# Kernel optimization log

Hardware: AMD Instinct MI355X
Metric: run time of the kernel (lower is better)

## Reference

```python
import jax, jax.numpy as jnp
import numpy as np

C = 256
C8 = C // 8

def setup_inputs() -> dict:
    key = jax.random.key(0)
    ks = jax.random.split(key, 8)
    B, H, W = 4, 64, 64
    x = jax.random.normal(ks[0], (B, C, H, W), dtype=jnp.float32)
    wq = jax.random.normal(ks[1], (C8, C), dtype=jnp.float32) * (1.0 / np.sqrt(C))
    bq = jnp.zeros((C8,), dtype=jnp.float32)
    wk = jax.random.normal(ks[2], (C8, C), dtype=jnp.float32) * (1.0 / np.sqrt(C))
    bk = jnp.zeros((C8,), dtype=jnp.float32)
    wv = jax.random.normal(ks[3], (C, C), dtype=jnp.float32) * (1.0 / np.sqrt(C))
    bv = jnp.zeros((C,), dtype=jnp.float32)
    gamma = jnp.ones((1,), dtype=jnp.float32) * 0.5  # nonzero so attention path contributes
    return {"x": x, "wq": wq, "bq": bq, "wk": wk, "bk": bk, "wv": wv, "bv": bv, "gamma": gamma}

def reference(x, wq, bq, wk, bk, wv, bv, gamma):
    B, Cc, Hh, Ww = x.shape
    N = Hh * Ww
    xf = x.reshape(B, Cc, N)  # [B,C,N]
    # 1x1 convs == per-pixel linear maps
    q = jnp.einsum('oc,bcn->bon', wq, xf) + bq[None, :, None]  # [B,C8,N]
    k = jnp.einsum('oc,bcn->bon', wk, xf) + bk[None, :, None]  # [B,C8,N]
    v = jnp.einsum('oc,bcn->bon', wv, xf) + bv[None, :, None]  # [B,C,N]
    # energy[b,n,m] = sum_c q[b,c,n] * k[b,c,m]  (unscaled)
    energy = jnp.einsum('bcn,bcm->bnm', q, k)
    attn = jax.nn.softmax(energy, axis=-1)
    # out[b,c,n] = sum_m v[b,c,m] * attn[b,n,m]
    out = jnp.einsum('bcm,bnm->bcn', v, attn).reshape(B, Cc, Hh, Ww)
    return gamma * out + x
```

## Files before the change

### kernel.cpp

```cpp
#include <hip/hip_runtime.h>
#include <hip/hip_fp16.h>

#define CC   256
#define QKC  32
#define NPIX 4096
#define NB   4
#define XSTR 264
#define VSTR 72
#define LOG2E 1.44269504088896340736f
#define TAU  8.0f

typedef __attribute__((ext_vector_type(8))) _Float16 f16x8;
typedef __attribute__((ext_vector_type(4))) float     f32x4;

static __device__ __forceinline__ unsigned h2bits(__half2 h) {
    union { __half2 h; unsigned u; } cv; cv.h = h; return cv.u;
}
#define E2(x) __builtin_amdgcn_exp2f(x)

__global__ __launch_bounds__(256) void wh_prep(
    const float* __restrict__ wq, const float* __restrict__ wk,
    const float* __restrict__ wv, __half* __restrict__ Wh)
{
    const int idx4 = blockIdx.x * 256 + threadIdx.x;
    const int o  = idx4 >> 6;
    const int cw = (idx4 & 63) << 2;
    const float* src;
    float scale = 1.0f;
    if (o < 256)      src = wv + (size_t)o * 256 + cw;
    else if (o < 288) { src = wq + (size_t)(o - 256) * 256 + cw; scale = LOG2E; }
    else              src = wk + (size_t)(o - 288) * 256 + cw;
    const float4 v = *reinterpret_cast<const float4*>(src);
    __half h[4] = {__float2half(v.x * scale), __float2half(v.y * scale),
                   __float2half(v.z * scale), __float2half(v.w * scale)};
    *reinterpret_cast<uint2*>(Wh + (size_t)o * 256 + cw) =
        *reinterpret_cast<const uint2*>(h);
}

__global__ __launch_bounds__(512) void qkv_mfma(
    const float* __restrict__ x, const __half* __restrict__ Wh,
    const float* __restrict__ bq, const float* __restrict__ bk,
    const float* __restrict__ bv,
    __half* __restrict__ Qh, __half* __restrict__ Kh, __half* __restrict__ VTh)
{
    __shared__ __align__(16) __half sm[CC * VSTR];
    __half* xT   = sm;
    __half* vres = sm;

    const int t  = threadIdx.x;
    const int b  = blockIdx.x >> 6;
    const int n0 = (blockIdx.x & 63) << 6;

    {
        const int nl4 = t & 15;
        const int c0  = t >> 4;
        const float* xp = x + ((size_t)b * CC) * NPIX + n0 + nl4 * 4;
        #pragma unroll
        for (int i = 0; i < 8; ++i) {
            const int c = c0 + 32 * i;
            const float4 v = *reinterpret_cast<const float4*>(xp + (size_t)c * NPIX);
            xT[(nl4 * 4 + 0) * XSTR + c] = __float2half(v.x);
            xT[(nl4 * 4 + 1) * XSTR + c] = __float2half(v.y);
            xT[(nl4 * 4 + 2) * XSTR + c] = __float2half(v.z);
            xT[(nl4 * 4 + 3) * XSTR + c] = __float2half(v.w);
        }
    }
    __syncthreads();

    const int w = t >> 6, l = t & 63, lr = l & 15, s = l >> 4;
    const int nto = (w < 4) ? 3 : 2;
    const int ob0 = 32 * w, ob1 = 32 * w + 16, ob2 = 256 + 16 * w;

    f16x8 wf[3][8];
    #pragma unroll
    for (int kk = 0; kk < 8; ++kk) {
        wf[0][kk] = *reinterpret_cast<const f16x8*>(
            Wh + (size_t)(ob0 + lr) * 256 + kk * 32 + s * 8);
        wf[1][kk] = *reinterpret_cast<const f16x8*>(
            Wh + (size_t)(ob1 + lr) * 256 + kk * 32 + s * 8);
    }
    if (w < 4)
        #pragma unroll
        for (int kk = 0; kk < 8; ++kk)
            wf[2][kk] = *reinterpret_cast<const f16x8*>(
                Wh + (size_t)(ob2 + lr) * 256 + kk * 32 + s * 8);

    f32x4 acc[3][4];
    #pragma unroll
    for (int j = 0; j < 3; ++j)
        #pragma unroll
        for (int nt = 0; nt < 4; ++nt) acc[j][nt] = (f32x4){0.f, 0.f, 0.f, 0.f};

    #pragma unroll
    for (int nt = 0; nt < 4; ++nt) {
        f16x8 xf[8];
        #pragma unroll
        for (int kk = 0; kk < 8; ++kk)
            xf[kk] = *reinterpret_cast<const f16x8*>(
                &xT[(nt * 16 + lr) * XSTR + kk * 32 + s * 8]);
        #pragma unroll
        for (int j = 0; j < 3; ++j)
            if (j < nto)
                #pragma unroll
                for (int kk = 0; kk < 8; ++kk)
                    acc[j][nt] = __builtin_amdgcn_mfma_f32_16x16x32_f16(
                        xf[kk], wf[j][kk], acc[j][nt], 0, 0, 0);
    }

    if (w < 4) {
        const bool is_q = (w < 2);
        const int oc = (w & 1) * 16 + lr;
        __half* dst = is_q ? Qh : Kh;
        const float bias = is_q ? bq[oc] * LOG2E : bk[oc];
        #pragma unroll
        for (int nt = 0; nt < 4; ++nt)
            #pragma unroll
            for (int r = 0; r < 4; ++r) {
                const size_t n = (size_t)b * NPIX + n0 + nt * 16 + s * 4 + r;
                dst[n * QKC + oc] = __float2half(acc[2][nt][r] + bias);
            }
    }

    __syncthreads();
    {
        #pragma unroll
        for (int j = 0; j < 2; ++j) {
            const int c = 32 * w + 16 * j + lr;
            const float bias = bv[c];
            #pragma unroll
            for (int nt = 0; nt < 4; ++nt) {
                __half h[4];
                #pragma unroll
                for (int r = 0; r < 4; ++r) h[r] = __float2half(acc[j][nt][r] + bias);
                *reinterpret_cast<uint2*>(&vres[c * VSTR + nt * 16 + s * 4]) =
                    *reinterpret_cast<const uint2*>(h);
            }
        }
    }
    __syncthreads();
    {
        const int c = t >> 1, half = t & 1;
        __half* dst = VTh + ((size_t)(b * CC + c)) * NPIX + n0 + half * 32;
        #pragma unroll
        for (int jj = 0; jj < 4; ++jj)
            *reinterpret_cast<uint4*>(dst + jj * 8) =
                *reinterpret_cast<const uint4*>(&vres[c * VSTR + half * 32 + jj * 8]);
    }
}

__global__ __launch_bounds__(512) void attn_mfma(
    const __half* __restrict__ Qh, const __half* __restrict__ Kh,
    const __half* __restrict__ VTh, const float* __restrict__ x,
    const float* __restrict__ gamma, float* __restrict__ out)
{
    __shared__ unsigned char Praw[2][64 * 128];
    __shared__ float abuf[2][64];
    __shared__ __align__(16) int fbuf[2][4];
    __shared__ float lbuf[64];

    const int t  = threadIdx.x;
    const int w  = t >> 6;
    const int l  = t & 63;
    const int lr = l & 15;
    const int s  = l >> 4;

    const int blk = (blockIdx.x & 7) * 32 + (blockIdx.x >> 3);
    const int b  = blk >> 6;
    const int n0 = (blk & 63) << 6;

    const int qw = w * 16 + lr;
    f16x8 qfrag;
    f16x8 kf[4];
    float m_run = -1e30f, l_run = 0.f;
    const __half* kbase = Kh + ((size_t)b * NPIX + lr) * QKC + s * 8;

    const int cbase = 64 * (w - 4);
    const __half* vbase = VTh + ((size_t)(b * CC + cbase + lr)) * NPIX + s * 8;
    f16x8 vA[4][2], vB[4][2];
    f32x4 O[4][4];
    #pragma unroll
    for (int ct = 0; ct < 4; ++ct)
        #pragma unroll
        for (int qt = 0; qt < 4; ++qt)
            O[ct][qt] = (f32x4){0.f, 0.f, 0.f, 0.f};

    auto do_softmax = [&](int bw) {
        f32x4 sacc[4];
        #pragma unroll
        for (int mt = 0; mt < 4; ++mt)
            sacc[mt] = __builtin_amdgcn_mfma_f32_16x16x32_f16(
                kf[mt], qfrag, (f32x4){0.f, 0.f, 0.f, 0.f}, 0, 0, 0);
        float v[16];
        #pragma unroll
        for (int mt = 0; mt < 4; ++mt)
            #pragma unroll
            for (int r = 0; r < 4; ++r) v[mt * 4 + r] = sacc[mt][r];
        float t8[8], t4[4], t2[2];
        #pragma unroll
        for (int i = 0; i < 8; ++i) t8[i] = fmaxf(v[i], v[i + 8]);
        #pragma unroll
        for (int i = 0; i < 4; ++i) t4[i] = fmaxf(t8[i], t8[i + 4]);
        t2[0] = fmaxf(t4[0], t4[2]); t2[1] = fmaxf(t4[1], t4[3]);
        const float m_l = fmaxf(t2[0], t2[1]);
        float p[16];
        #pragma unroll
        for (int i = 0; i < 16; ++i) p[i] = E2(v[i] - m_l);
        float s8[8], s4[4], s2[2];
        #pragma unroll
        for (int i = 0; i < 8; ++i) s8[i] = p[i] + p[i + 8];
        #pragma unroll
        for (int i = 0; i < 4; ++i) s4[i] = s8[i] + s8[i + 4];
        s2[0] = s4[0] + s4[2]; s2[1] = s4[1] + s4[3];
        const float e_l = s2[0] + s2[1];
        float m_p = __shfl_xor(m_l, 16);
        float e_p = __shfl_xor(e_l, 16);
        const float m1 = fmaxf(m_l, m_p);
        const float e1 = e_l * E2(m_l - m1) + e_p * E2(m_p - m1);
        m_p = __shfl_xor(m1, 32);
        e_p = __shfl_xor(e1, 32);
        const float m_g = fmaxf(m1, m_p);
        const float e_g = e1 * E2(m1 - m_g) + e_p * E2(m_p - m_g);
        const bool need = (m_g - m_run) > TAU;
        float f;
        if (__any(need)) {
            const float mnew = fmaxf(m_run, m_g);
            const float al   = E2(m_run - mnew);
            l_run = al * l_run + e_g * E2(m_g - mnew);
            f = E2(m_l - mnew);
            if (l < 16) abuf[bw][qw] = al;
            if (l == 0) fbuf[bw][w] = 1;
            m_run = mnew;
        } else {
            l_run += e_g * E2(m_g - m_run);
            f = E2(m_l - m_run);
            if (l < 16) abuf[bw][qw] = 1.0f;
            if (l == 0) fbuf[bw][w] = 0;
        }
        unsigned char* pb = &Praw[bw][0];
        #pragma unroll
        for (int mt = 0; mt < 4; ++mt) {
            const int g = ((s >> 1) + 2 * mt) ^ (qw & 7);
            uint2 u;
            u.x = h2bits(__floats2half2_rn(p[mt * 4 + 0] * f, p[mt * 4 + 1] * f));
            u.y = h2bits(__floats2half2_rn(p[mt * 4 + 2] * f, p[mt * 4 + 3] * f));
            *reinterpret_cast<uint2*>(pb + qw * 128 + g * 16 + (s & 1) * 8) = u;
        }
    };

    auto vload = [&](f16x8 (&dst)[4][2], int m0) {
        #pragma unroll
        for (int ct = 0; ct < 4; ++ct)
            #pragma unroll
            for (int ks = 0; ks < 2; ++ks)
                dst[ct][ks] = *reinterpret_cast<const f16x8*>(
                    vbase + (size_t)ct * 16 * NPIX + m0 + ks * 32);
    };

    auto pv_body = [&](int pbuf, f16x8 (&vf)[4][2]) {
        const int4 fl = *reinterpret_cast<const int4*>(&fbuf[pbuf][0]);
        if (fl.x | fl.y | fl.z | fl.w) {
            float av[4];
            #pragma unroll
            for (int qt = 0; qt < 4; ++qt) av[qt] = abuf[pbuf][qt * 16 + lr];
            #pragma unroll
            for (int ct = 0; ct < 4; ++ct)
                #pragma unroll
                for (int qt = 0; qt < 4; ++qt)
                    #pragma unroll
                    for (int r = 0; r < 4; ++r) O[ct][qt][r] *= av[qt];
        }
        const unsigned char* pr = &Praw[pbuf][0];
        __builtin_amdgcn_s_setprio(1);
        #pragma unroll
        for (int qt = 0; qt < 4; ++qt) {
            const int q2 = qt * 16 + lr;
            const int g0 = s ^ (q2 & 7);
            const int g1 = (s + 4) ^ (q2 & 7);
            const f16x8 pf0 = *reinterpret_cast<const f16x8*>(pr + q2 * 128 + g0 * 16);
            const f16x8 pf1 = *reinterpret_cast<const f16x8*>(pr + q2 * 128 + g1 * 16);
            #pragma unroll
            for (int ct = 0; ct < 4; ++ct) {
                O[ct][qt] = __builtin_amdgcn_mfma_f32_16x16x32_f16(
                    vf[ct][0], pf0, O[ct][qt], 0, 0, 0);
                O[ct][qt] = __builtin_amdgcn_mfma_f32_16x16x32_f16(
                    vf[ct][1], pf1, O[ct][qt], 0, 0, 0);
            }
        }
        __builtin_amdgcn_s_setprio(0);
    };

    if (w < 4) {
        qfrag = *reinterpret_cast<const f16x8*>(
            Qh + ((size_t)b * NPIX + n0 + qw) * QKC + s * 8);
        #pragma unroll
        for (int mt = 0; mt < 4; ++mt)
            kf[mt] = *reinterpret_cast<const f16x8*>(kbase + (size_t)(mt * 16) * QKC);
        do_softmax(0);
        #pragma unroll
        for (int mt = 0; mt < 4; ++mt)
            kf[mt] = *reinterpret_cast<const f16x8*>(kbase + (size_t)(64 + mt * 16) * QKC);
    } else {
        vload(vA, 0);
    }
    __syncthreads();

    for (int it = 0; it < 32; ++it) {
        const int se = 2 * it;
        if (w < 4) {
            do_softmax(1);
            if (se < 62) {
                const size_t moff = (size_t)((se + 2) * 64) * QKC;
                #pragma unroll
                for (int mt = 0; mt < 4; ++mt)
                    kf[mt] = *reinterpret_cast<const f16x8*>(
                        kbase + moff + (size_t)(mt * 16) * QKC);
            }
        } else {
            vload(vB, (se + 1) * 64);
            pv_body(0, vA);
        }
        __syncthreads();
        const int so = se + 1;
        if (w < 4) {
            if (so < 63) {
                do_softmax(0);
                if (so < 62) {
                    const size_t moff = (size_t)((so + 2) * 64) * QKC;
                    #pragma unroll
                    for (int mt = 0; mt < 4; ++mt)
                        kf[mt] = *reinterpret_cast<const f16x8*>(
                            kbase + moff + (size_t)(mt * 16) * QKC);
                }
            }
        } else {
            if (so < 63) vload(vA, (so + 1) * 64);
            pv_body(1, vB);
        }
        __syncthreads();
    }

    if (w < 4) { if (l < 16) lbuf[qw] = l_run; }
    __syncthreads();
    if (w >= 4) {
        const float g = gamma[0];
        float linv[4];
        #pragma unroll
        for (int qt = 0; qt < 4; ++qt) linv[qt] = g / lbuf[qt * 16 + lr];
        #pragma unroll
        for (int ct = 0; ct < 4; ++ct)
            #pragma unroll
            for (int qt = 0; qt < 4; ++qt)
                #pragma unroll
                for (int r = 0; r < 4; ++r) {
                    const int c = cbase + ct * 16 + s * 4 + r;
                    const size_t idx = ((size_t)(b * CC + c)) * NPIX + n0 + qt * 16 + lr;
                    out[idx] = O[ct][qt][r] * linv[qt] + x[idx];
                }
    }
}

extern "C" void kernel_launch(void* const* d_in, const int* in_sizes, int n_in,
                              void* d_out, int out_size, void* d_ws, size_t ws_size,
                              hipStream_t stream) {
    const float* x     = (const float*)d_in[0];
    const float* wq    = (const float*)d_in[1];
    const float* bq    = (const float*)d_in[2];
    const float* wk    = (const float*)d_in[3];
    const float* bk    = (const float*)d_in[4];
    const float* wv    = (const float*)d_in[5];
    const float* bv    = (const float*)d_in[6];
    const float* gamma = (const float*)d_in[7];
    float* out = (float*)d_out;

    __half* Wh  = (__half*)d_ws;
    __half* Qh  = Wh + (size_t)320 * 256;
    __half* Kh  = Qh + (size_t)NB * NPIX * QKC;
    __half* VTh = Kh + (size_t)NB * NPIX * QKC;

    hipLaunchKernelGGL(wh_prep, dim3(80), dim3(256), 0, stream, wq, wk, wv, Wh);
    hipLaunchKernelGGL(qkv_mfma, dim3(NB * 64), dim3(512), 0, stream,
                       x, Wh, bq, bk, bv, Qh, Kh, VTh);
    hipLaunchKernelGGL(attn_mfma, dim3(256), dim3(512), 0, stream,
                       Qh, Kh, VTh, x, gamma, out);
}
```

Baseline: 108.2 us.

## Split PV work across eight consumer waves with 128-key softmax intervals

```diff
diff --git a/kernel.cpp b/kernel.cpp
--- a/kernel.cpp
+++ b/kernel.cpp
@@ -7,6 +7,7 @@
 #define NB   4
 #define XSTR 264
 #define VSTR 72
+#define OSTR 68
 #define LOG2E 1.44269504088896340736f
 #define TAU  8.0f
 
@@ -148,15 +149,18 @@
     }
 }
 
-__global__ __launch_bounds__(512) void attn_mfma(
+__global__ __launch_bounds__(768, 3) void attn_mfma(
     const __half* __restrict__ Qh, const __half* __restrict__ Kh,
     const __half* __restrict__ VTh, const float* __restrict__ x,
     const float* __restrict__ gamma, float* __restrict__ out)
 {
-    __shared__ unsigned char Praw[2][64 * 128];
+    __shared__ __align__(16) unsigned char smraw[4 * 64 * OSTR * 4];
     __shared__ float abuf[2][64];
     __shared__ __align__(16) int fbuf[2][4];
     __shared__ float lbuf[64];
+
+    unsigned char* const Praw = smraw;
+    float* const Ocomb = reinterpret_cast<float*>(smraw);
 
     const int t  = threadIdx.x;
     const int w  = t >> 6;
@@ -170,13 +174,14 @@
 
     const int qw = w * 16 + lr;
     f16x8 qfrag;
-    f16x8 kf[4];
+    f16x8 kfA[4], kfB[4];
     float m_run = -1e30f, l_run = 0.f;
     const __half* kbase = Kh + ((size_t)b * NPIX + lr) * QKC + s * 8;
 
-    const int cbase = 64 * (w - 4);
-    const __half* vbase = VTh + ((size_t)(b * CC + cbase + lr)) * NPIX + s * 8;
-    f16x8 vA[4][2], vB[4][2];
+    const int wid = w - 4;
+    const int cg  = wid & 3;
+    const int mh  = wid >> 2;
+    const __half* vbase = VTh + ((size_t)(b * CC + cg * 64 + lr)) * NPIX + s * 8;
     f32x4 O[4][4];
     #pragma unroll
     for (int ct = 0; ct < 4; ++ct)
@@ -184,84 +189,108 @@
         for (int qt = 0; qt < 4; ++qt)
             O[ct][qt] = (f32x4){0.f, 0.f, 0.f, 0.f};
 
-    auto do_softmax = [&](int bw) {
-        f32x4 sacc[4];
+    auto ldk = [&](f16x8 (&dst)[4], int tile) {
+        const size_t off = (size_t)(tile * 64) * QKC;
         #pragma unroll
         for (int mt = 0; mt < 4; ++mt)
-            sacc[mt] = __builtin_amdgcn_mfma_f32_16x16x32_f16(
-                kf[mt], qfrag, (f32x4){0.f, 0.f, 0.f, 0.f}, 0, 0, 0);
-        float v[16];
+            dst[mt] = *reinterpret_cast<const f16x8*>(
+                kbase + off + (size_t)(mt * 16) * QKC);
+    };
+
+    auto do_interval = [&](int i, int bw) {
+        f32x4 sa[4], sb[4];
         #pragma unroll
         for (int mt = 0; mt < 4; ++mt)
-            #pragma unroll
-            for (int r = 0; r < 4; ++r) v[mt * 4 + r] = sacc[mt][r];
-        float t8[8], t4[4], t2[2];
-        #pragma unroll
-        for (int i = 0; i < 8; ++i) t8[i] = fmaxf(v[i], v[i + 8]);
-        #pragma unroll
-        for (int i = 0; i < 4; ++i) t4[i] = fmaxf(t8[i], t8[i + 4]);
-        t2[0] = fmaxf(t4[0], t4[2]); t2[1] = fmaxf(t4[1], t4[3]);
-        const float m_l = fmaxf(t2[0], t2[1]);
-        float p[16];
-        #pragma unroll
-        for (int i = 0; i < 16; ++i) p[i] = E2(v[i] - m_l);
-        float s8[8], s4[4], s2[2];
-        #pragma unroll
-        for (int i = 0; i < 8; ++i) s8[i] = p[i] + p[i + 8];
-        #pragma unroll
-        for (int i = 0; i < 4; ++i) s4[i] = s8[i] + s8[i + 4];
-        s2[0] = s4[0] + s4[2]; s2[1] = s4[1] + s4[3];
-        const float e_l = s2[0] + s2[1];
-        float m_p = __shfl_xor(m_l, 16);
-        float e_p = __shfl_xor(e_l, 16);
-        const float m1 = fmaxf(m_l, m_p);
-        const float e1 = e_l * E2(m_l - m1) + e_p * E2(m_p - m1);
+            sa[mt] = __builtin_amdgcn_mfma_f32_16x16x32_f16(
+                kfA[mt], qfrag, (f32x4){0.f, 0.f, 0.f, 0.f}, 0, 0, 0);
+        #pragma unroll
+        for (int mt = 0; mt < 4; ++mt)
+            sb[mt] = __builtin_amdgcn_mfma_f32_16x16x32_f16(
+                kfB[mt], qfrag, (f32x4){0.f, 0.f, 0.f, 0.f}, 0, 0, 0);
+        if (i < 31) { ldk(kfA, 2 * i + 2); ldk(kfB, 2 * i + 3); }
+
+        float va[16], vb[16];
+        #pragma unroll
+        for (int mt = 0; mt < 4; ++mt)
+            #pragma unroll
+            for (int r = 0; r < 4; ++r) {
+                va[mt * 4 + r] = sa[mt][r];
+                vb[mt * 4 + r] = sb[mt][r];
+            }
+        float ta[8], tb[8];
+        #pragma unroll
+        for (int i2 = 0; i2 < 8; ++i2) { ta[i2] = fmaxf(va[i2], va[i2+8]); tb[i2] = fmaxf(vb[i2], vb[i2+8]); }
+        float ta4[4], tb4[4];
+        #pragma unroll
+        for (int i2 = 0; i2 < 4; ++i2) { ta4[i2] = fmaxf(ta[i2], ta[i2+4]); tb4[i2] = fmaxf(tb[i2], tb[i2+4]); }
+        const float m_lA = fmaxf(fmaxf(ta4[0], ta4[2]), fmaxf(ta4[1], ta4[3]));
+        const float m_lB = fmaxf(fmaxf(tb4[0], tb4[2]), fmaxf(tb4[1], tb4[3]));
+        float pa[16], pb[16];
+        #pragma unroll
+        for (int i2 = 0; i2 < 16; ++i2) { pa[i2] = E2(va[i2] - m_lA); pb[i2] = E2(vb[i2] - m_lB); }
+        float sa8[8], sb8[8];
+        #pragma unroll
+        for (int i2 = 0; i2 < 8; ++i2) { sa8[i2] = pa[i2] + pa[i2+8]; sb8[i2] = pb[i2] + pb[i2+8]; }
+        float sa4[4], sb4[4];
+        #pragma unroll
+        for (int i2 = 0; i2 < 4; ++i2) { sa4[i2] = sa8[i2] + sa8[i2+4]; sb4[i2] = sb8[i2] + sb8[i2+4]; }
+        const float e_lA = (sa4[0] + sa4[2]) + (sa4[1] + sa4[3]);
+        const float e_lB = (sb4[0] + sb4[2]) + (sb4[1] + sb4[3]);
+        const float m_ab = fmaxf(m_lA, m_lB);
+        const float e_ab = e_lA * E2(m_lA - m_ab) + e_lB * E2(m_lB - m_ab);
+        float m_p = __shfl_xor(m_ab, 16);
+        float e_p = __shfl_xor(e_ab, 16);
+        const float m1 = fmaxf(m_ab, m_p);
+        const float e1 = e_ab * E2(m_ab - m1) + e_p * E2(m_p - m1);
         m_p = __shfl_xor(m1, 32);
         e_p = __shfl_xor(e1, 32);
         const float m_g = fmaxf(m1, m_p);
         const float e_g = e1 * E2(m1 - m_g) + e_p * E2(m_p - m_g);
         const bool need = (m_g - m_run) > TAU;
-        float f;
+        float fA, fB;
         if (__any(need)) {
             const float mnew = fmaxf(m_run, m_g);
             const float al   = E2(m_run - mnew);
             l_run = al * l_run + e_g * E2(m_g - mnew);
-            f = E2(m_l - mnew);
+            fA = E2(m_lA - mnew); fB = E2(m_lB - mnew);
             if (l < 16) abuf[bw][qw] = al;
             if (l == 0) fbuf[bw][w] = 1;
             m_run = mnew;
         } else {
             l_run += e_g * E2(m_g - m_run);
-            f = E2(m_l - m_run);
+            fA = E2(m_lA - m_run); fB = E2(m_lB - m_run);
             if (l < 16) abuf[bw][qw] = 1.0f;
             if (l == 0) fbuf[bw][w] = 0;
         }
-        unsigned char* pb = &Praw[bw][0];
+        unsigned char* pbA = Praw + bw * 16384;
+        unsigned char* pbB = pbA + 8192;
         #pragma unroll
         for (int mt = 0; mt < 4; ++mt) {
             const int g = ((s >> 1) + 2 * mt) ^ (qw & 7);
-            uint2 u;
-            u.x = h2bits(__floats2half2_rn(p[mt * 4 + 0] * f, p[mt * 4 + 1] * f));
-            u.y = h2bits(__floats2half2_rn(p[mt * 4 + 2] * f, p[mt * 4 + 3] * f));
-            *reinterpret_cast<uint2*>(pb + qw * 128 + g * 16 + (s & 1) * 8) = u;
+            uint2 ua, ub;
+            ua.x = h2bits(__floats2half2_rn(pa[mt*4+0] * fA, pa[mt*4+1] * fA));
+            ua.y = h2bits(__floats2half2_rn(pa[mt*4+2] * fA, pa[mt*4+3] * fA));
+            ub.x = h2bits(__floats2half2_rn(pb[mt*4+0] * fB, pb[mt*4+1] * fB));
+            ub.y = h2bits(__floats2half2_rn(pb[mt*4+2] * fB, pb[mt*4+3] * fB));
+            *reinterpret_cast<uint2*>(pbA + qw * 128 + g * 16 + (s & 1) * 8) = ua;
+            *reinterpret_cast<uint2*>(pbB + qw * 128 + g * 16 + (s & 1) * 8) = ub;
         }
     };
 
-    auto vload = [&](f16x8 (&dst)[4][2], int m0) {
+    auto pv = [&](int i, int bw) {
+        const int m0 = i * 128 + mh * 64;
+        f16x8 vf[4][2];
         #pragma unroll
         for (int ct = 0; ct < 4; ++ct)
             #pragma unroll
             for (int ks = 0; ks < 2; ++ks)
-                dst[ct][ks] = *reinterpret_cast<const f16x8*>(
+                vf[ct][ks] = *reinterpret_cast<const f16x8*>(
                     vbase + (size_t)ct * 16 * NPIX + m0 + ks * 32);
-    };
-
-    auto pv_body = [&](int pbuf, f16x8 (&vf)[4][2]) {
-        const int4 fl = *reinterpret_cast<const int4*>(&fbuf[pbuf][0]);
+        const int4 fl = *reinterpret_cast<const int4*>(&fbuf[bw][0]);
         if (fl.x | fl.y | fl.z | fl.w) {
             float av[4];
             #pragma unroll
-            for (int qt = 0; qt < 4; ++qt) av[qt] = abuf[pbuf][qt * 16 + lr];
+            for (int qt = 0; qt < 4; ++qt) av[qt] = abuf[bw][qt * 16 + lr];
             #pragma unroll
             for (int ct = 0; ct < 4; ++ct)
                 #pragma unroll
@@ -269,7 +298,7 @@
                     #pragma unroll
                     for (int r = 0; r < 4; ++r) O[ct][qt][r] *= av[qt];
         }
-        const unsigned char* pr = &Praw[pbuf][0];
+        const unsigned char* pr = Praw + bw * 16384 + mh * 8192;
         __builtin_amdgcn_s_setprio(1);
         #pragma unroll
         for (int qt = 0; qt < 4; ++qt) {
@@ -292,69 +321,50 @@
     if (w < 4) {
         qfrag = *reinterpret_cast<const f16x8*>(
             Qh + ((size_t)b * NPIX + n0 + qw) * QKC + s * 8);
-        #pragma unroll
-        for (int mt = 0; mt < 4; ++mt)
-            kf[mt] = *reinterpret_cast<const f16x8*>(kbase + (size_t)(mt * 16) * QKC);
-        do_softmax(0);
-        #pragma unroll
-        for (int mt = 0; mt < 4; ++mt)
-            kf[mt] = *reinterpret_cast<const f16x8*>(kbase + (size_t)(64 + mt * 16) * QKC);
-    } else {
-        vload(vA, 0);
+        ldk(kfA, 0); ldk(kfB, 1);
+        do_interval(0, 0);
     }
     __syncthreads();
 
     for (int it = 0; it < 32; ++it) {
-        const int se = 2 * it;
         if (w < 4) {
-            do_softmax(1);
-            if (se < 62) {
-                const size_t moff = (size_t)((se + 2) * 64) * QKC;
-                #pragma unroll
-                for (int mt = 0; mt < 4; ++mt)
-                    kf[mt] = *reinterpret_cast<const f16x8*>(
-                        kbase + moff + (size_t)(mt * 16) * QKC);
-            }
+            if (it < 31) do_interval(it + 1, (it + 1) & 1);
         } else {
-            vload(vB, (se + 1) * 64);
-            pv_body(0, vA);
+            pv(it, it & 1);
         }
         __syncthreads();
-        const int so = se + 1;
-        if (w < 4) {
-            if (so < 63) {
-                do_softmax(0);
-                if (so < 62) {
-                    const size_t moff = (size_t)((so + 2) * 64) * QKC;
-                    #pragma unroll
-                    for (int mt = 0; mt < 4; ++mt)
-                        kf[mt] = *reinterpret_cast<const f16x8*>(
-                            kbase + moff + (size_t)(mt * 16) * QKC);
-                }
-            }
-        } else {
-            if (so < 63) vload(vA, (so + 1) * 64);
-            pv_body(1, vB);
-        }
-        __syncthreads();
-    }
-
-    if (w < 4) { if (l < 16) lbuf[qw] = l_run; }
-    __syncthreads();
-    if (w >= 4) {
+    }
+
+    if (w < 4) {
+        if (l < 16) lbuf[qw] = l_run;
+    } else if (mh == 1) {
+        float* oc = Ocomb + cg * 64 * OSTR;
+        #pragma unroll
+        for (int ct = 0; ct < 4; ++ct)
+            #pragma unroll
+            for (int qt = 0; qt < 4; ++qt)
+                #pragma unroll
+                for (int r = 0; r < 4; ++r)
+                    oc[(ct * 16 + s * 4 + r) * OSTR + qt * 16 + lr] = O[ct][qt][r];
+    }
+    __syncthreads();
+    if (w >= 4 && mh == 0) {
         const float g = gamma[0];
         float linv[4];
         #pragma unroll
         for (int qt = 0; qt < 4; ++qt) linv[qt] = g / lbuf[qt * 16 + lr];
+        const float* oc = Ocomb + cg * 64 * OSTR;
         #pragma unroll
         for (int ct = 0; ct < 4; ++ct)
             #pragma unroll
             for (int qt = 0; qt < 4; ++qt)
                 #pragma unroll
                 for (int r = 0; r < 4; ++r) {
-                    const int c = cbase + ct * 16 + s * 4 + r;
+                    const int c = cg * 64 + ct * 16 + s * 4 + r;
                     const size_t idx = ((size_t)(b * CC + c)) * NPIX + n0 + qt * 16 + lr;
-                    out[idx] = O[ct][qt][r] * linv[qt] + x[idx];
+                    const float o2 = O[ct][qt][r] +
+                                     oc[(ct * 16 + s * 4 + r) * OSTR + qt * 16 + lr];
+                    out[idx] = o2 * linv[qt] + x[idx];
                 }
     }
 }
@@ -380,6 +390,6 @@
     hipLaunchKernelGGL(wh_prep, dim3(80), dim3(256), 0, stream, wq, wk, wv, Wh);
     hipLaunchKernelGGL(qkv_mfma, dim3(NB * 64), dim3(512), 0, stream,
                        x, Wh, bq, bk, bv, Qh, Kh, VTh);
-    hipLaunchKernelGGL(attn_mfma, dim3(256), dim3(512), 0, stream,
+    hipLaunchKernelGGL(attn_mfma, dim3(256), dim3(768), 0, stream,
                        Qh, Kh, VTh, x, gamma, out);
 }
```

After: 156.1 us. 44.4% more time.

## Split attention over key range into two halves with a combine kernel

Applied to the files above, without the earlier changes.

```diff
diff --git a/kernel.cpp b/kernel.cpp
--- a/kernel.cpp
+++ b/kernel.cpp
@@ -148,10 +148,10 @@
     }
 }
 
-__global__ __launch_bounds__(512) void attn_mfma(
+__global__ __launch_bounds__(512, 4) void attn_partial(
     const __half* __restrict__ Qh, const __half* __restrict__ Kh,
-    const __half* __restrict__ VTh, const float* __restrict__ x,
-    const float* __restrict__ gamma, float* __restrict__ out)
+    const __half* __restrict__ VTh, float2* __restrict__ ML,
+    __half* __restrict__ Oc1, float* __restrict__ out)
 {
     __shared__ unsigned char Praw[2][64 * 128];
     __shared__ float abuf[2][64];
@@ -164,18 +164,19 @@
     const int lr = l & 15;
     const int s  = l >> 4;
 
-    const int blk = (blockIdx.x & 7) * 32 + (blockIdx.x >> 3);
-    const int b  = blk >> 6;
-    const int n0 = (blk & 63) << 6;
+    const int lb = (blockIdx.x & 7) * 64 + (blockIdx.x >> 3);
+    const int h  = lb >> 8;
+    const int b  = (lb >> 6) & 3;
+    const int n0 = (lb & 63) << 6;
 
     const int qw = w * 16 + lr;
     f16x8 qfrag;
     f16x8 kf[4];
     float m_run = -1e30f, l_run = 0.f;
-    const __half* kbase = Kh + ((size_t)b * NPIX + lr) * QKC + s * 8;
+    const __half* kbase = Kh + ((size_t)b * NPIX + h * 2048 + lr) * QKC + s * 8;
 
     const int cbase = 64 * (w - 4);
-    const __half* vbase = VTh + ((size_t)(b * CC + cbase + lr)) * NPIX + s * 8;
+    const __half* vbase = VTh + ((size_t)(b * CC + cbase + lr)) * NPIX + h * 2048 + s * 8;
     f16x8 vA[4][2], vB[4][2];
     f32x4 O[4][4];
     #pragma unroll
@@ -184,6 +185,14 @@
         for (int qt = 0; qt < 4; ++qt)
             O[ct][qt] = (f32x4){0.f, 0.f, 0.f, 0.f};
 
+    auto ldk = [&](int tile) {
+        const size_t off = (size_t)(tile * 64) * QKC;
+        #pragma unroll
+        for (int mt = 0; mt < 4; ++mt)
+            kf[mt] = *reinterpret_cast<const f16x8*>(
+                kbase + off + (size_t)(mt * 16) * QKC);
+    };
+
     auto do_softmax = [&](int bw) {
         f32x4 sacc[4];
         #pragma unroll
@@ -195,23 +204,21 @@
         for (int mt = 0; mt < 4; ++mt)
             #pragma unroll
             for (int r = 0; r < 4; ++r) v[mt * 4 + r] = sacc[mt][r];
-        float t8[8], t4[4], t2[2];
+        float t8[8], t4[4];
         #pragma unroll
         for (int i = 0; i < 8; ++i) t8[i] = fmaxf(v[i], v[i + 8]);
         #pragma unroll
         for (int i = 0; i < 4; ++i) t4[i] = fmaxf(t8[i], t8[i + 4]);
-        t2[0] = fmaxf(t4[0], t4[2]); t2[1] = fmaxf(t4[1], t4[3]);
-        const float m_l = fmaxf(t2[0], t2[1]);
+        const float m_l = fmaxf(fmaxf(t4[0], t4[2]), fmaxf(t4[1], t4[3]));
         float p[16];
         #pragma unroll
         for (int i = 0; i < 16; ++i) p[i] = E2(v[i] - m_l);
-        float s8[8], s4[4], s2[2];
+        float s8[8], s4[4];
         #pragma unroll
         for (int i = 0; i < 8; ++i) s8[i] = p[i] + p[i + 8];
         #pragma unroll
         for (int i = 0; i < 4; ++i) s4[i] = s8[i] + s8[i + 4];
-        s2[0] = s4[0] + s4[2]; s2[1] = s4[1] + s4[3];
-        const float e_l = s2[0] + s2[1];
+        const float e_l = (s4[0] + s4[2]) + (s4[1] + s4[3]);
         float m_p = __shfl_xor(m_l, 16);
         float e_p = __shfl_xor(e_l, 16);
         const float m1 = fmaxf(m_l, m_p);
@@ -289,74 +296,126 @@
         __builtin_amdgcn_s_setprio(0);
     };
 
+    #define STEP_BARRIER(IS_S)                                    \
+        { if (IS_S) asm volatile("s_waitcnt lgkmcnt(0)" ::: "memory"); \
+          __builtin_amdgcn_sched_barrier(0);                      \
+          __builtin_amdgcn_s_barrier();                           \
+          __builtin_amdgcn_sched_barrier(0); }
+
     if (w < 4) {
         qfrag = *reinterpret_cast<const f16x8*>(
             Qh + ((size_t)b * NPIX + n0 + qw) * QKC + s * 8);
-        #pragma unroll
-        for (int mt = 0; mt < 4; ++mt)
-            kf[mt] = *reinterpret_cast<const f16x8*>(kbase + (size_t)(mt * 16) * QKC);
+        ldk(0);
         do_softmax(0);
-        #pragma unroll
-        for (int mt = 0; mt < 4; ++mt)
-            kf[mt] = *reinterpret_cast<const f16x8*>(kbase + (size_t)(64 + mt * 16) * QKC);
+        ldk(1);
+        STEP_BARRIER(true)
     } else {
         vload(vA, 0);
-    }
-    __syncthreads();
-
-    for (int it = 0; it < 32; ++it) {
+        STEP_BARRIER(false)
+    }
+
+    for (int it = 0; it < 16; ++it) {
         const int se = 2 * it;
         if (w < 4) {
             do_softmax(1);
-            if (se < 62) {
-                const size_t moff = (size_t)((se + 2) * 64) * QKC;
-                #pragma unroll
-                for (int mt = 0; mt < 4; ++mt)
-                    kf[mt] = *reinterpret_cast<const f16x8*>(
-                        kbase + moff + (size_t)(mt * 16) * QKC);
-            }
+            if (se < 30) ldk(se + 2);
+            STEP_BARRIER(true)
         } else {
             vload(vB, (se + 1) * 64);
             pv_body(0, vA);
-        }
-        __syncthreads();
+            STEP_BARRIER(false)
+        }
         const int so = se + 1;
         if (w < 4) {
-            if (so < 63) {
+            if (so < 31) {
                 do_softmax(0);
-                if (so < 62) {
-                    const size_t moff = (size_t)((so + 2) * 64) * QKC;
-                    #pragma unroll
-                    for (int mt = 0; mt < 4; ++mt)
-                        kf[mt] = *reinterpret_cast<const f16x8*>(
-                            kbase + moff + (size_t)(mt * 16) * QKC);
-                }
+                if (so < 30) ldk(so + 2);
             }
+            STEP_BARRIER(true)
         } else {
-            if (so < 63) vload(vA, (so + 1) * 64);
+            if (so < 31) vload(vA, (so + 1) * 64);
             pv_body(1, vB);
-        }
-        __syncthreads();
-    }
-
-    if (w < 4) { if (l < 16) lbuf[qw] = l_run; }
+            STEP_BARRIER(false)
+        }
+    }
+    #undef STEP_BARRIER
+
+    if (w < 4) {
+        if (l < 16) {
+            lbuf[qw] = l_run;
+            ML[(size_t)h * NB * NPIX + (size_t)b * NPIX + n0 + qw] =
+                make_float2(m_run, l_run);
+        }
+    }
     __syncthreads();
     if (w >= 4) {
-        const float g = gamma[0];
         float linv[4];
         #pragma unroll
-        for (int qt = 0; qt < 4; ++qt) linv[qt] = g / lbuf[qt * 16 + lr];
-        #pragma unroll
-        for (int ct = 0; ct < 4; ++ct)
-            #pragma unroll
-            for (int qt = 0; qt < 4; ++qt)
+        for (int qt = 0; qt < 4; ++qt) linv[qt] = 1.0f / lbuf[qt * 16 + lr];
+        if (h == 0) {
+            #pragma unroll
+            for (int ct = 0; ct < 4; ++ct)
                 #pragma unroll
-                for (int r = 0; r < 4; ++r) {
-                    const int c = cbase + ct * 16 + s * 4 + r;
-                    const size_t idx = ((size_t)(b * CC + c)) * NPIX + n0 + qt * 16 + lr;
-                    out[idx] = O[ct][qt][r] * linv[qt] + x[idx];
-                }
-    }
+                for (int qt = 0; qt < 4; ++qt)
+                    #pragma unroll
+                    for (int r = 0; r < 4; ++r) {
+                        const int c = cbase + ct * 16 + s * 4 + r;
+                        const size_t idx = ((size_t)(b * CC + c)) * NPIX + n0 + qt * 16 + lr;
+                        out[idx] = O[ct][qt][r] * linv[qt];
+                    }
+        } else {
+            #pragma unroll
+            for (int ct = 0; ct < 4; ++ct)
+                #pragma unroll
+                for (int qt = 0; qt < 4; ++qt)
+                    #pragma unroll
+                    for (int r = 0; r < 4; ++r) {
+                        const int c = cbase + ct * 16 + s * 4 + r;
+                        const size_t idx = ((size_t)(b * CC + c)) * NPIX + n0 + qt * 16 + lr;
+                        Oc1[idx] = __float2half(O[ct][qt][r] * linv[qt]);
+                    }
+        }
+    }
+}
+
+__global__ __launch_bounds__(256) void combine(
+    const __half* __restrict__ Oc1, const float2* __restrict__ ML,
+    const float* __restrict__ x, const float* __restrict__ gamma,
+    float* __restrict__ out)
+{
+    const int gid = blockIdx.x * 256 + threadIdx.x;
+    const int row = gid >> 9;
+    const int n8  = (gid & 511) << 3;
+    const int b   = row >> 8;
+    const size_t base = (size_t)row * NPIX + n8;
+    const float g = gamma[0];
+
+    const float4 o0a = *reinterpret_cast<const float4*>(out + base);
+    const float4 o0b = *reinterpret_cast<const float4*>(out + base + 4);
+    const uint4  u1  = *reinterpret_cast<const uint4*>(Oc1 + base);
+    const float4 xa  = *reinterpret_cast<const float4*>(x + base);
+    const float4 xb  = *reinterpret_cast<const float4*>(x + base + 4);
+
+    union { uint4 u; __half h[8]; } cv; cv.u = u1;
+    float o0[8] = {o0a.x, o0a.y, o0a.z, o0a.w, o0b.x, o0b.y, o0b.z, o0b.w};
+    float xv[8] = {xa.x, xa.y, xa.z, xa.w, xb.x, xb.y, xb.z, xb.w};
+
+    const float2* ml0 = ML + (size_t)b * NPIX + n8;
+    const float2* ml1 = ML + (size_t)NB * NPIX + (size_t)b * NPIX + n8;
+
+    float res[8];
+    #pragma unroll
+    for (int j = 0; j < 8; ++j) {
+        const float2 a = ml0[j];
+        const float2 c2 = ml1[j];
+        const float ms = fmaxf(a.x, c2.x);
+        const float w0 = a.y * E2(a.x - ms);
+        const float w1 = c2.y * E2(c2.x - ms);
+        const float o = (w0 * o0[j] + w1 * __half2float(cv.h[j])) / (w0 + w1);
+        res[j] = g * o + xv[j];
+    }
+    *reinterpret_cast<float4*>(out + base)     = make_float4(res[0], res[1], res[2], res[3]);
+    *reinterpret_cast<float4*>(out + base + 4) = make_float4(res[4], res[5], res[6], res[7]);
 }
 
 extern "C" void kernel_launch(void* const* d_in, const int* in_sizes, int n_in,
@@ -376,10 +435,14 @@
     __half* Qh  = Wh + (size_t)320 * 256;
     __half* Kh  = Qh + (size_t)NB * NPIX * QKC;
     __half* VTh = Kh + (size_t)NB * NPIX * QKC;
+    __half* Oc1 = VTh + (size_t)NB * NPIX * CC;
+    float2* ML  = (float2*)(Oc1 + (size_t)NB * NPIX * CC);
 
     hipLaunchKernelGGL(wh_prep, dim3(80), dim3(256), 0, stream, wq, wk, wv, Wh);
     hipLaunchKernelGGL(qkv_mfma, dim3(NB * 64), dim3(512), 0, stream,
                        x, Wh, bq, bk, bv, Qh, Kh, VTh);
-    hipLaunchKernelGGL(attn_mfma, dim3(256), dim3(512), 0, stream,
-                       Qh, Kh, VTh, x, gamma, out);
-}
+    hipLaunchKernelGGL(attn_partial, dim3(512), dim3(512), 0, stream,
+                       Qh, Kh, VTh, ML, Oc1, out);
+    hipLaunchKernelGGL(combine, dim3(2048), dim3(256), 0, stream,
+                       Oc1, ML, x, gamma, out);
+}
```

Result: slower. 315.3 us (+191.4%).

## Fuse softmax and PV into every wave, removing producer/consumer barriers

Applied to the files above, without the earlier changes.

```diff
diff --git a/kernel.cpp b/kernel.cpp
--- a/kernel.cpp
+++ b/kernel.cpp
@@ -148,214 +148,175 @@
     }
 }
 
-__global__ __launch_bounds__(512) void attn_mfma(
+__global__ __launch_bounds__(512) void attn_fused(
     const __half* __restrict__ Qh, const __half* __restrict__ Kh,
     const __half* __restrict__ VTh, const float* __restrict__ x,
     const float* __restrict__ gamma, float* __restrict__ out)
 {
-    __shared__ unsigned char Praw[2][64 * 128];
-    __shared__ float abuf[2][64];
-    __shared__ __align__(16) int fbuf[2][4];
-    __shared__ float lbuf[64];
+    __shared__ unsigned char Praw[8][4096];
 
     const int t  = threadIdx.x;
     const int w  = t >> 6;
     const int l  = t & 63;
     const int lr = l & 15;
     const int s  = l >> 4;
-
-    const int blk = (blockIdx.x & 7) * 32 + (blockIdx.x >> 3);
-    const int b  = blk >> 6;
-    const int n0 = (blk & 63) << 6;
-
-    const int qw = w * 16 + lr;
-    f16x8 qfrag;
+    const int qt2 = w >> 2;
+    const int ch  = w & 3;
+
+    const int lb = (blockIdx.x & 7) * 32 + (blockIdx.x >> 3);
+    const int b  = lb >> 6;
+    const int n0 = (lb & 63) << 6;
+    const int q0 = n0 + qt2 * 32;
+    const int cb = ch * 64;
+
+    unsigned char* const pb = &Praw[w][0];
+
+    f16x8 qf[2];
+    #pragma unroll
+    for (int sub = 0; sub < 2; ++sub)
+        qf[sub] = *reinterpret_cast<const f16x8*>(
+            Qh + ((size_t)b * NPIX + q0 + sub * 16 + lr) * QKC + s * 8);
+
+    const __half* kbase = Kh + ((size_t)b * NPIX + lr) * QKC + s * 8;
+    const __half* vbase = VTh + ((size_t)(b * CC + cb + lr)) * NPIX + s * 8;
+
     f16x8 kf[4];
-    float m_run = -1e30f, l_run = 0.f;
-    const __half* kbase = Kh + ((size_t)b * NPIX + lr) * QKC + s * 8;
-
-    const int cbase = 64 * (w - 4);
-    const __half* vbase = VTh + ((size_t)(b * CC + cbase + lr)) * NPIX + s * 8;
-    f16x8 vA[4][2], vB[4][2];
-    f32x4 O[4][4];
+    f16x8 vf[4][2];
+    f32x4 O[2][4];
+    float m_run[2] = {-1e30f, -1e30f};
+    float l_run[2] = {0.f, 0.f};
+    #pragma unroll
+    for (int sub = 0; sub < 2; ++sub)
+        #pragma unroll
+        for (int ct = 0; ct < 4; ++ct)
+            O[sub][ct] = (f32x4){0.f, 0.f, 0.f, 0.f};
+
+    #pragma unroll
+    for (int mt = 0; mt < 4; ++mt)
+        kf[mt] = *reinterpret_cast<const f16x8*>(kbase + (size_t)(mt * 16) * QKC);
     #pragma unroll
     for (int ct = 0; ct < 4; ++ct)
         #pragma unroll
-        for (int qt = 0; qt < 4; ++qt)
-            O[ct][qt] = (f32x4){0.f, 0.f, 0.f, 0.f};
-
-    auto do_softmax = [&](int bw) {
-        f32x4 sacc[4];
-        #pragma unroll
-        for (int mt = 0; mt < 4; ++mt)
-            sacc[mt] = __builtin_amdgcn_mfma_f32_16x16x32_f16(
-                kf[mt], qfrag, (f32x4){0.f, 0.f, 0.f, 0.f}, 0, 0, 0);
-        float v[16];
-        #pragma unroll
-        for (int mt = 0; mt < 4; ++mt)
-            #pragma unroll
-            for (int r = 0; r < 4; ++r) v[mt * 4 + r] = sacc[mt][r];
-        float t8[8], t4[4], t2[2];
-        #pragma unroll
-        for (int i = 0; i < 8; ++i) t8[i] = fmaxf(v[i], v[i + 8]);
-        #pragma unroll
-        for (int i = 0; i < 4; ++i) t4[i] = fmaxf(t8[i], t8[i + 4]);
-        t2[0] = fmaxf(t4[0], t4[2]); t2[1] = fmaxf(t4[1], t4[3]);
-        const float m_l = fmaxf(t2[0], t2[1]);
-        float p[16];
-        #pragma unroll
-        for (int i = 0; i < 16; ++i) p[i] = E2(v[i] - m_l);
-        float s8[8], s4[4], s2[2];
-        #pragma unroll
-        for (int i = 0; i < 8; ++i) s8[i] = p[i] + p[i + 8];
-        #pragma unroll
-        for (int i = 0; i < 4; ++i) s4[i] = s8[i] + s8[i + 4];
-        s2[0] = s4[0] + s4[2]; s2[1] = s4[1] + s4[3];
-        const float e_l = s2[0] + s2[1];
-        float m_p = __shfl_xor(m_l, 16);
-        float e_p = __shfl_xor(e_l, 16);
-        const float m1 = fmaxf(m_l, m_p);
-        const float e1 = e_l * E2(m_l - m1) + e_p * E2(m_p - m1);
-        m_p = __shfl_xor(m1, 32);
-        e_p = __shfl_xor(e1, 32);
-        const float m_g = fmaxf(m1, m_p);
-        const float e_g = e1 * E2(m1 - m_g) + e_p * E2(m_p - m_g);
-        const bool need = (m_g - m_run) > TAU;
-        float f;
-        if (__any(need)) {
-            const float mnew = fmaxf(m_run, m_g);
-            const float al   = E2(m_run - mnew);
-            l_run = al * l_run + e_g * E2(m_g - mnew);
-            f = E2(m_l - mnew);
-            if (l < 16) abuf[bw][qw] = al;
-            if (l == 0) fbuf[bw][w] = 1;
-            m_run = mnew;
-        } else {
-            l_run += e_g * E2(m_g - m_run);
-            f = E2(m_l - m_run);
-            if (l < 16) abuf[bw][qw] = 1.0f;
-            if (l == 0) fbuf[bw][w] = 0;
-        }
-        unsigned char* pb = &Praw[bw][0];
-        #pragma unroll
-        for (int mt = 0; mt < 4; ++mt) {
-            const int g = ((s >> 1) + 2 * mt) ^ (qw & 7);
-            uint2 u;
-            u.x = h2bits(__floats2half2_rn(p[mt * 4 + 0] * f, p[mt * 4 + 1] * f));
-            u.y = h2bits(__floats2half2_rn(p[mt * 4 + 2] * f, p[mt * 4 + 3] * f));
-            *reinterpret_cast<uint2*>(pb + qw * 128 + g * 16 + (s & 1) * 8) = u;
-        }
-    };
-
-    auto vload = [&](f16x8 (&dst)[4][2], int m0) {
-        #pragma unroll
-        for (int ct = 0; ct < 4; ++ct)
-            #pragma unroll
-            for (int ks = 0; ks < 2; ++ks)
-                dst[ct][ks] = *reinterpret_cast<const f16x8*>(
-                    vbase + (size_t)ct * 16 * NPIX + m0 + ks * 32);
-    };
-
-    auto pv_body = [&](int pbuf, f16x8 (&vf)[4][2]) {
-        const int4 fl = *reinterpret_cast<const int4*>(&fbuf[pbuf][0]);
-        if (fl.x | fl.y | fl.z | fl.w) {
-            float av[4];
-            #pragma unroll
-            for (int qt = 0; qt < 4; ++qt) av[qt] = abuf[pbuf][qt * 16 + lr];
-            #pragma unroll
-            for (int ct = 0; ct < 4; ++ct)
-                #pragma unroll
-                for (int qt = 0; qt < 4; ++qt)
+        for (int kc = 0; kc < 2; ++kc)
+            vf[ct][kc] = *reinterpret_cast<const f16x8*>(
+                vbase + (size_t)ct * 16 * NPIX + kc * 32);
+
+    for (int it = 0; it < 64; ++it) {
+        f32x4 sacc[2][4];
+        #pragma unroll
+        for (int sub = 0; sub < 2; ++sub)
+            #pragma unroll
+            for (int mt = 0; mt < 4; ++mt)
+                sacc[sub][mt] = __builtin_amdgcn_mfma_f32_16x16x32_f16(
+                    kf[mt], qf[sub], (f32x4){0.f, 0.f, 0.f, 0.f}, 0, 0, 0);
+
+        {
+            const size_t moff = (size_t)(((it + 1) & 63) * 64) * QKC;
+            #pragma unroll
+            for (int mt = 0; mt < 4; ++mt)
+                kf[mt] = *reinterpret_cast<const f16x8*>(
+                    kbase + moff + (size_t)(mt * 16) * QKC);
+        }
+
+        #pragma unroll
+        for (int sub = 0; sub < 2; ++sub) {
+            float v[16];
+            #pragma unroll
+            for (int mt = 0; mt < 4; ++mt)
+                #pragma unroll
+                for (int r = 0; r < 4; ++r) v[mt * 4 + r] = sacc[sub][mt][r];
+            float t8[8], t4[4];
+            #pragma unroll
+            for (int i = 0; i < 8; ++i) t8[i] = fmaxf(v[i], v[i + 8]);
+            #pragma unroll
+            for (int i = 0; i < 4; ++i) t4[i] = fmaxf(t8[i], t8[i + 4]);
+            const float m_l = fmaxf(fmaxf(t4[0], t4[2]), fmaxf(t4[1], t4[3]));
+            float p[16];
+            #pragma unroll
+            for (int i = 0; i < 16; ++i) p[i] = E2(v[i] - m_l);
+            float s8[8], s4[4];
+            #pragma unroll
+            for (int i = 0; i < 8; ++i) s8[i] = p[i] + p[i + 8];
+            #pragma unroll
+            for (int i = 0; i < 4; ++i) s4[i] = s8[i] + s8[i + 4];
+            const float e_l = (s4[0] + s4[2]) + (s4[1] + s4[3]);
+            float m_p = __shfl_xor(m_l, 16);
+            float e_p = __shfl_xor(e_l, 16);
+            const float m1 = fmaxf(m_l, m_p);
+            const float e1 = e_l * E2(m_l - m1) + e_p * E2(m_p - m1);
+            m_p = __shfl_xor(m1, 32);
+            e_p = __shfl_xor(e1, 32);
+            const float m_g = fmaxf(m1, m_p);
+            const float e_g = e1 * E2(m1 - m_g) + e_p * E2(m_p - m_g);
+
+            const bool need = (m_g - m_run[sub]) > TAU;
+            float f;
+            if (__any(need)) {
+                const float mnew = fmaxf(m_run[sub], m_g);
+                const float al   = E2(m_run[sub] - mnew);
+                l_run[sub] = al * l_run[sub] + e_g * E2(m_g - mnew);
+                f = E2(m_l - mnew);
+                m_run[sub] = mnew;
+                #pragma unroll
+                for (int ct = 0; ct < 4; ++ct)
                     #pragma unroll
-                    for (int r = 0; r < 4; ++r) O[ct][qt][r] *= av[qt];
-        }
-        const unsigned char* pr = &Praw[pbuf][0];
+                    for (int r = 0; r < 4; ++r) O[sub][ct][r] *= al;
+            } else {
+                l_run[sub] += e_g * E2(m_g - m_run[sub]);
+                f = E2(m_l - m_run[sub]);
+            }
+            const int qw = sub * 16 + lr;
+            #pragma unroll
+            for (int mt = 0; mt < 4; ++mt) {
+                const int g = ((s >> 1) + 2 * mt) ^ (qw & 7);
+                uint2 u;
+                u.x = h2bits(__floats2half2_rn(p[mt * 4 + 0] * f, p[mt * 4 + 1] * f));
+                u.y = h2bits(__floats2half2_rn(p[mt * 4 + 2] * f, p[mt * 4 + 3] * f));
+                *reinterpret_cast<uint2*>(pb + qw * 128 + g * 16 + (s & 1) * 8) = u;
+            }
+        }
+
         __builtin_amdgcn_s_setprio(1);
         #pragma unroll
-        for (int qt = 0; qt < 4; ++qt) {
-            const int q2 = qt * 16 + lr;
+        for (int sub = 0; sub < 2; ++sub) {
+            const int q2 = sub * 16 + lr;
             const int g0 = s ^ (q2 & 7);
             const int g1 = (s + 4) ^ (q2 & 7);
-            const f16x8 pf0 = *reinterpret_cast<const f16x8*>(pr + q2 * 128 + g0 * 16);
-            const f16x8 pf1 = *reinterpret_cast<const f16x8*>(pr + q2 * 128 + g1 * 16);
+            const f16x8 pf0 = *reinterpret_cast<const f16x8*>(pb + q2 * 128 + g0 * 16);
+            const f16x8 pf1 = *reinterpret_cast<const f16x8*>(pb + q2 * 128 + g1 * 16);
             #pragma unroll
             for (int ct = 0; ct < 4; ++ct) {
-                O[ct][qt] = __builtin_amdgcn_mfma_f32_16x16x32_f16(
-                    vf[ct][0], pf0, O[ct][qt], 0, 0, 0);
-                O[ct][qt] = __builtin_amdgcn_mfma_f32_16x16x32_f16(
-                    vf[ct][1], pf1, O[ct][qt], 0, 0, 0);
+                O[sub][ct] = __builtin_amdgcn_mfma_f32_16x16x32_f16(
+                    vf[ct][0], pf0, O[sub][ct], 0, 0, 0);
+                O[sub][ct] = __builtin_amdgcn_mfma_f32_16x16x32_f16(
+                    vf[ct][1], pf1, O[sub][ct], 0, 0, 0);
             }
         }
         __builtin_amdgcn_s_setprio(0);
-    };
-
-    if (w < 4) {
-        qfrag = *reinterpret_cast<const f16x8*>(
-            Qh + ((size_t)b * NPIX + n0 + qw) * QKC + s * 8);
-        #pragma unroll
-        for (int mt = 0; mt < 4; ++mt)
-            kf[mt] = *reinterpret_cast<const f16x8*>(kbase + (size_t)(mt * 16) * QKC);
-        do_softmax(0);
-        #pragma unroll
-        for (int mt = 0; mt < 4; ++mt)
-            kf[mt] = *reinterpret_cast<const f16x8*>(kbase + (size_t)(64 + mt * 16) * QKC);
-    } else {
-        vload(vA, 0);
-    }
-    __syncthreads();
-
-    for (int it = 0; it < 32; ++it) {
-        const int se = 2 * it;
-        if (w < 4) {
-            do_softmax(1);
-            if (se < 62) {
-                const size_t moff = (size_t)((se + 2) * 64) * QKC;
-                #pragma unroll
-                for (int mt = 0; mt < 4; ++mt)
-                    kf[mt] = *reinterpret_cast<const f16x8*>(
-                        kbase + moff + (size_t)(mt * 16) * QKC);
-            }
-        } else {
-            vload(vB, (se + 1) * 64);
-            pv_body(0, vA);
-        }
-        __syncthreads();
-        const int so = se + 1;
-        if (w < 4) {
-            if (so < 63) {
-                do_softmax(0);
-                if (so < 62) {
-                    const size_t moff = (size_t)((so + 2) * 64) * QKC;
-                    #pragma unroll
-                    for (int mt = 0; mt < 4; ++mt)
-                        kf[mt] = *reinterpret_cast<const f16x8*>(
-                            kbase + moff + (size_t)(mt * 16) * QKC);
-                }
-            }
-        } else {
-            if (so < 63) vload(vA, (so + 1) * 64);
-            pv_body(1, vB);
-        }
-        __syncthreads();
-    }
-
-    if (w < 4) { if (l < 16) lbuf[qw] = l_run; }
-    __syncthreads();
-    if (w >= 4) {
-        const float g = gamma[0];
-        float linv[4];
-        #pragma unroll
-        for (int qt = 0; qt < 4; ++qt) linv[qt] = g / lbuf[qt * 16 + lr];
+
+        {
+            const int m0 = ((it + 1) & 63) * 64;
+            #pragma unroll
+            for (int ct = 0; ct < 4; ++ct)
+                #pragma unroll
+                for (int kc = 0; kc < 2; ++kc)
+                    vf[ct][kc] = *reinterpret_cast<const f16x8*>(
+                        vbase + (size_t)ct * 16 * NPIX + m0 + kc * 32);
+        }
+    }
+
+    const float g = gamma[0];
+    #pragma unroll
+    for (int sub = 0; sub < 2; ++sub) {
+        const float linv = g / l_run[sub];
         #pragma unroll
         for (int ct = 0; ct < 4; ++ct)
             #pragma unroll
-            for (int qt = 0; qt < 4; ++qt)
-                #pragma unroll
-                for (int r = 0; r < 4; ++r) {
-                    const int c = cbase + ct * 16 + s * 4 + r;
-                    const size_t idx = ((size_t)(b * CC + c)) * NPIX + n0 + qt * 16 + lr;
-                    out[idx] = O[ct][qt][r] * linv[qt] + x[idx];
-                }
+            for (int r = 0; r < 4; ++r) {
+                const int c = cb + ct * 16 + s * 4 + r;
+                const size_t idx = ((size_t)(b * CC + c)) * NPIX + q0 + sub * 16 + lr;
+                out[idx] = O[sub][ct][r] * linv + x[idx];
+            }
     }
 }
 
@@ -380,6 +341,6 @@
     hipLaunchKernelGGL(wh_prep, dim3(80), dim3(256), 0, stream, wq, wk, wv, Wh);
     hipLaunchKernelGGL(qkv_mfma, dim3(NB * 64), dim3(512), 0, stream,
                        x, Wh, bq, bk, bv, Qh, Kh, VTh);
-    hipLaunchKernelGGL(attn_mfma, dim3(256), dim3(512), 0, stream,
+    hipLaunchKernelGGL(attn_fused, dim3(256), dim3(512), 0, stream,
                        Qh, Kh, VTh, x, gamma, out);
 }
```

Result: slower. 170.1 us (+57.3%).
